# Optimization experiments

Hardware: AMD Instinct MI355X
Metric: run time of the kernel (lower is better)

## Reference

```python
import jax, jax.numpy as jnp
import numpy as np

H_DIM, HEAD_DIM, N_HEADS = 1024, 64, 16
B, S = 4, 2048

def phi(x):
    return jax.nn.elu(x) + 1.0

def setup_inputs() -> dict:
    key = jax.random.key(0)
    ks = jax.random.split(key, 14)
    std = 0.02
    inp = {
        'query': jax.random.normal(ks[0], (B, S, H_DIM), jnp.float32),
        'key':   jax.random.normal(ks[1], (B, S, H_DIM), jnp.float32),
        'value': jax.random.normal(ks[2], (B, S, H_DIM), jnp.float32),
        'beta':  jax.random.normal(ks[3], (B, S, H_DIM), jnp.float32),
        # torch nn.Linear convention: W is [out, in]
        'Wq': std * jax.random.normal(ks[4], (N_HEADS * HEAD_DIM, H_DIM), jnp.float32),
        'bq': jnp.zeros((N_HEADS * HEAD_DIM,), jnp.float32),
        'Wk': std * jax.random.normal(ks[5], (N_HEADS * HEAD_DIM, H_DIM), jnp.float32),
        'bk': jnp.zeros((N_HEADS * HEAD_DIM,), jnp.float32),
        'Wv': std * jax.random.normal(ks[6], (N_HEADS * HEAD_DIM, H_DIM), jnp.float32),
        'bv': jnp.zeros((N_HEADS * HEAD_DIM,), jnp.float32),
        'Wb': std * jax.random.normal(ks[7], (N_HEADS, H_DIM), jnp.float32),
        'bb': jnp.zeros((N_HEADS,), jnp.float32),
        'Wo': std * jax.random.normal(ks[8], (H_DIM, N_HEADS * HEAD_DIM), jnp.float32),
        'bo': jnp.zeros((H_DIM,), jnp.float32),
    }
    return inp

def reference(query, key, value, beta, Wq, bq, Wk, bk, Wv, bv, Wb, bb, Wo, bo):
    bsz, seqlen, _ = query.shape
    q = query @ Wq.T + bq            # [B,S,H*D]
    k = key   @ Wk.T + bk
    v = value @ Wv.T + bv
    b = jax.nn.sigmoid(beta @ Wb.T + bb)  # [B,S,H]

    def heads(x):  # [B,S,H*D] -> [B,H,S,D]
        return x.reshape(bsz, seqlen, N_HEADS, HEAD_DIM).transpose(0, 2, 1, 3)
    q, k, v = heads(q), heads(k), heads(v)
    b = b.transpose(0, 2, 1)              # [B,H,S]

    phi_q, phi_k = phi(q), phi(k)

    # NOTE: the original uses torch.einsum('bhdd,bhd->bhd', W, x), whose repeated
    # subscript takes the DIAGONAL of W. The recurrence thus reduces exactly to a
    # d-vector diagonal state: s <- s + beta*(v - s*pk)*pk ; y = s_new * pq.
    def step(s, xs):
        pk_t, pq_t, v_t, b_t = xs          # [B,H,D],[B,H,D],[B,H,D],[B,H]
        v_bar = s * pk_t                   # diag(prev_W) @ phi_k  == elementwise
        bdv = b_t[..., None] * (v_t - v_bar)
        s_new = s + bdv * pk_t             # diagonal of prev_W + outer(bdv, pk)
        y = s_new * pq_t                   # diag(curr_W) * phi_q
        return s_new, y

    # time-major scan inputs: [S,B,H,D]
    xs = (phi_k.transpose(2, 0, 1, 3), phi_q.transpose(2, 0, 1, 3),
          v.transpose(2, 0, 1, 3), b.transpose(2, 0, 1))
    s0 = jnp.zeros((bsz, N_HEADS, HEAD_DIM), query.dtype)
    _, ys = jax.lax.scan(step, s0, xs)     # ys: [S,B,H,D]

    out = ys.transpose(1, 0, 2, 3).reshape(bsz, seqlen, N_HEADS * HEAD_DIM)
    return out @ Wo.T + bo
```

## Files before the change

kernel.cpp:

```cpp
#include <hip/hip_runtime.h>
#include <cstdint>
#include <cstddef>

#define H_DIM 1024
#define HEADS 16
#define HD 64
#define BATCH 4
#define SEQ 2048
#define M_ROWS (BATCH*SEQ)

typedef __bf16 bf16x8 __attribute__((ext_vector_type(8)));
typedef float floatx4 __attribute__((ext_vector_type(4)));
typedef unsigned short ushortx8 __attribute__((ext_vector_type(8)));

__device__ __forceinline__ unsigned short f2bf(float f) {
    union { float f; uint32_t u; } c; c.f = f;
    uint32_t u = c.u;
    u += 0x7fffu + ((u >> 16) & 1u);
    return (unsigned short)(u >> 16);
}
__device__ __forceinline__ float bf2f(unsigned short h) {
    union { uint32_t u; float f; } c; c.u = ((uint32_t)h) << 16;
    return c.f;
}

#define GLD_LDS16(gp, lp) \
    __builtin_amdgcn_global_load_lds((__attribute__((address_space(1))) void*)(gp), \
                                     (__attribute__((address_space(3))) void*)(lp), 16, 0, 0)

__global__ __launch_bounds__(256) void cast_bf16(const float* __restrict__ in,
                                                 unsigned short* __restrict__ out)
{
    size_t i = (size_t)blockIdx.x * 256 + threadIdx.x;
    const float4* p = (const float4*)in;
    float4 a = p[i * 2], b = p[i * 2 + 1];
    ushortx8 o;
    o[0] = f2bf(a.x); o[1] = f2bf(a.y); o[2] = f2bf(a.z); o[3] = f2bf(a.w);
    o[4] = f2bf(b.x); o[5] = f2bf(b.y); o[6] = f2bf(b.z); o[7] = f2bf(b.w);
    *(ushortx8*)(out + i * 8) = o;
}

enum { EPI_NONE = 0, EPI_PHI = 1 };

__device__ __forceinline__ void store_out(float* C, size_t idx, float x) { C[idx] = x; }
__device__ __forceinline__ void store_out(unsigned short* C, size_t idx, float x) { C[idx] = f2bf(x); }

template<int EPI, typename OutT>
__global__ __launch_bounds__(256) void gemm_mfma(const unsigned short* __restrict__ A,
                                                 const unsigned short* __restrict__ W,
                                                 const float* __restrict__ bias,
                                                 OutT* __restrict__ C,
                                                 int M, int N, int K)
{
    constexpr int TM = 128, TN = 128, TK = 32;
    __shared__ __align__(16) unsigned short Ast[TM * TK];
    __shared__ __align__(16) unsigned short Bst[TN * TK];

    const int tid  = threadIdx.x;
    const int wave = tid >> 6;
    const int lane = tid & 63;
    const int bm = blockIdx.y * TM;
    const int bn = blockIdx.x * TN;

    const int srow  = wave * 16 + (lane >> 2);
    const int skoff = (lane & 3) * 8;

    const int wm   = (wave & 1) * 64;
    const int wn   = (wave >> 1) * 64;
    const int quad = lane >> 4;
    const int l16  = lane & 15;

    floatx4 acc[4][4] = {};

    const unsigned short* Abase = A + (size_t)bm * K;
    const unsigned short* Wbase = W + (size_t)bn * K;

    for (int k0 = 0; k0 < K; k0 += TK) {
        __syncthreads();
        GLD_LDS16(Abase + (size_t)srow        * K + k0 + skoff, &Ast[(wave * 16)      * TK]);
        GLD_LDS16(Abase + (size_t)(srow + 64) * K + k0 + skoff, &Ast[(64 + wave * 16) * TK]);
        GLD_LDS16(Wbase + (size_t)srow        * K + k0 + skoff, &Bst[(wave * 16)      * TK]);
        GLD_LDS16(Wbase + (size_t)(srow + 64) * K + k0 + skoff, &Bst[(64 + wave * 16) * TK]);
        __syncthreads();

        bf16x8 af[4], bfr[4];
        #pragma unroll
        for (int i = 0; i < 4; ++i)
            af[i] = *(const bf16x8*)&Ast[(wm + i * 16 + l16) * TK + quad * 8];
        #pragma unroll
        for (int j = 0; j < 4; ++j)
            bfr[j] = *(const bf16x8*)&Bst[(wn + j * 16 + l16) * TK + quad * 8];
        #pragma unroll
        for (int i = 0; i < 4; ++i)
            #pragma unroll
            for (int j = 0; j < 4; ++j)
                acc[i][j] = __builtin_amdgcn_mfma_f32_16x16x32_bf16(af[i], bfr[j], acc[i][j], 0, 0, 0);
    }

    #pragma unroll
    for (int i = 0; i < 4; ++i) {
        #pragma unroll
        for (int j = 0; j < 4; ++j) {
            const int col = bn + wn + j * 16 + l16;
            const float bval = bias[col];
            #pragma unroll
            for (int r = 0; r < 4; ++r) {
                const int row = bm + wm + i * 16 + quad * 4 + r;
                float x = acc[i][j][r] + bval;
                if (EPI == EPI_PHI) x = (x > 0.f) ? (x + 1.f) : __expf(x);
                store_out(C, (size_t)row * N + col, x);
            }
        }
    }
}

__global__ __launch_bounds__(256) void proj_b(const float* __restrict__ beta,
                                              const float* __restrict__ Wb,
                                              const float* __restrict__ bbias,
                                              float* __restrict__ bout)
{
    const int wave = threadIdx.x >> 6;
    const int lane = threadIdx.x & 63;
    const int m = blockIdx.x * 4 + wave;

    const float4* brow = (const float4*)(beta + (size_t)m * H_DIM);
    const float4* wb4  = (const float4*)Wb;

    float acc[16];
    #pragma unroll
    for (int n = 0; n < 16; ++n) acc[n] = 0.f;

    #pragma unroll
    for (int j = 0; j < 4; ++j) {
        float4 a = brow[j * 64 + lane];
        #pragma unroll
        for (int n = 0; n < 16; ++n) {
            float4 w = wb4[n * 256 + j * 64 + lane];
            acc[n] = fmaf(a.x, w.x, acc[n]);
            acc[n] = fmaf(a.y, w.y, acc[n]);
            acc[n] = fmaf(a.z, w.z, acc[n]);
            acc[n] = fmaf(a.w, w.w, acc[n]);
        }
    }

    #pragma unroll
    for (int n = 0; n < 16; ++n) {
        float s = acc[n];
        s += __shfl_xor(s, 32);
        s += __shfl_xor(s, 16);
        s += __shfl_xor(s, 8);
        s += __shfl_xor(s, 4);
        s += __shfl_xor(s, 2);
        s += __shfl_xor(s, 1);
        acc[n] = s;
    }

    float sel = acc[0];
    #pragma unroll
    for (int n = 1; n < 16; ++n)
        sel = (lane == n) ? acc[n] : sel;
    if (lane < 16) {
        float s = sel + bbias[lane];
        bout[(size_t)m * HEADS + lane] = 1.f / (1.f + __expf(-s));
    }
}

constexpr int NCHUNK = 64;
constexpr int CLEN   = SEQ / NCHUNK;
constexpr int NGH    = BATCH * HEADS * HD;

__global__ __launch_bounds__(256) void scan_phase1(const unsigned short* __restrict__ pk_,
                                                   const unsigned short* __restrict__ v_,
                                                   const float* __restrict__ b_,
                                                   float* __restrict__ Aarr,
                                                   float* __restrict__ Carr)
{
    const int idx   = blockIdx.x * 256 + threadIdx.x;
    const int d     = idx & 63;
    const int h     = (idx >> 6) & 15;
    const int bb    = (idx >> 10) & 3;
    const int chunk = idx >> 12;
    const int g     = idx & (NGH - 1);
    const int t0    = chunk * CLEN;

    const unsigned short* pkp = pk_ + (size_t)bb * SEQ * H_DIM + h * HD + d + (size_t)t0 * H_DIM;
    const unsigned short* vp  = v_  + (size_t)bb * SEQ * H_DIM + h * HD + d + (size_t)t0 * H_DIM;
    const float*          bp  = b_  + (size_t)bb * SEQ * HEADS + h        + (size_t)t0 * HEADS;

    float A = 1.f, C = 0.f;
    #pragma unroll 8
    for (int t = 0; t < CLEN; ++t) {
        float pk = bf2f(pkp[(size_t)t * H_DIM]);
        float vv = bf2f(vp[(size_t)t * H_DIM]);
        float bt = bp[(size_t)t * HEADS];
        float a  = 1.f - bt * pk * pk;
        float c  = bt * vv * pk;
        A *= a;
        C = fmaf(a, C, c);
    }
    Aarr[(size_t)chunk * NGH + g] = A;
    Carr[(size_t)chunk * NGH + g] = C;
}

__global__ __launch_bounds__(256) void scan_phase2(const float* __restrict__ Aarr,
                                                   const float* __restrict__ Carr,
                                                   float* __restrict__ S0)
{
    const int g = blockIdx.x * 256 + threadIdx.x;
    float s = 0.f;
    #pragma unroll
    for (int c = 0; c < NCHUNK; ++c) {
        S0[(size_t)c * NGH + g] = s;
        s = fmaf(Aarr[(size_t)c * NGH + g], s, Carr[(size_t)c * NGH + g]);
    }
}

__global__ __launch_bounds__(256) void scan_phase3(const unsigned short* __restrict__ pk_,
                                                   unsigned short* __restrict__ pq_,
                                                   const unsigned short* __restrict__ v_,
                                                   const float* __restrict__ b_,
                                                   const float* __restrict__ S0)
{
    const int idx   = blockIdx.x * 256 + threadIdx.x;
    const int d     = idx & 63;
    const int h     = (idx >> 6) & 15;
    const int bb    = (idx >> 10) & 3;
    const int chunk = idx >> 12;
    const int g     = idx & (NGH - 1);
    const int t0    = chunk * CLEN;

    const unsigned short* pkp = pk_ + (size_t)bb * SEQ * H_DIM + h * HD + d + (size_t)t0 * H_DIM;
    unsigned short*       pqp = pq_ + (size_t)bb * SEQ * H_DIM + h * HD + d + (size_t)t0 * H_DIM;
    const unsigned short* vp  = v_  + (size_t)bb * SEQ * H_DIM + h * HD + d + (size_t)t0 * H_DIM;
    const float*          bp  = b_  + (size_t)bb * SEQ * HEADS + h        + (size_t)t0 * HEADS;

    float s = S0[(size_t)chunk * NGH + g];
    #pragma unroll 8
    for (int t = 0; t < CLEN; ++t) {
        float pk = bf2f(pkp[(size_t)t * H_DIM]);
        float pq = bf2f(pqp[(size_t)t * H_DIM]);
        float vv = bf2f(vp[(size_t)t * H_DIM]);
        float bt = bp[(size_t)t * HEADS];
        float bdv = bt * (vv - s * pk);
        s = fmaf(bdv, pk, s);
        pqp[(size_t)t * H_DIM] = f2bf(s * pq);
    }
}

extern "C" void kernel_launch(void* const* d_in, const int* in_sizes, int n_in,
                              void* d_out, int out_size, void* d_ws, size_t ws_size,
                              hipStream_t stream)
{
    const float* query = (const float*)d_in[0];
    const float* key   = (const float*)d_in[1];
    const float* value = (const float*)d_in[2];
    const float* beta  = (const float*)d_in[3];
    const float* Wq    = (const float*)d_in[4];
    const float* bq    = (const float*)d_in[5];
    const float* Wk    = (const float*)d_in[6];
    const float* bk    = (const float*)d_in[7];
    const float* Wv    = (const float*)d_in[8];
    const float* bv    = (const float*)d_in[9];
    const float* Wb    = (const float*)d_in[10];
    const float* bbias = (const float*)d_in[11];
    const float* Wo    = (const float*)d_in[12];
    const float* bo    = (const float*)d_in[13];
    float* out = (float*)d_out;

    const size_t ACT = (size_t)M_ROWS * H_DIM;
    const size_t WEL = (size_t)H_DIM * H_DIM;

    unsigned short* ws = (unsigned short*)d_ws;
    unsigned short* Xbf    = ws;
    unsigned short* phi_q  = ws + ACT;
    unsigned short* phi_k  = ws + 2 * ACT;
    unsigned short* vbuf   = ws + 3 * ACT;
    unsigned short* Wq_bf  = ws + 4 * ACT;
    unsigned short* Wk_bf  = Wq_bf + WEL;
    unsigned short* Wv_bf  = Wk_bf + WEL;
    unsigned short* Wo_bf  = Wv_bf + WEL;
    float*          bbuf   = (float*)(Wo_bf + WEL);
    float*          Aarr   = bbuf + (size_t)M_ROWS * HEADS;
    float*          Carr   = Aarr + (size_t)NCHUNK * NGH;
    float*          S0     = Carr + (size_t)NCHUNK * NGH;

    const int ACT_CAST_BLOCKS = (int)(ACT / (8 * 256));
    const int W_CAST_BLOCKS   = (int)(WEL / (8 * 256));

    cast_bf16<<<W_CAST_BLOCKS, 256, 0, stream>>>(Wq, Wq_bf);
    cast_bf16<<<W_CAST_BLOCKS, 256, 0, stream>>>(Wk, Wk_bf);
    cast_bf16<<<W_CAST_BLOCKS, 256, 0, stream>>>(Wv, Wv_bf);
    cast_bf16<<<W_CAST_BLOCKS, 256, 0, stream>>>(Wo, Wo_bf);

    dim3 ggrid(H_DIM / 128, M_ROWS / 128);

    cast_bf16<<<ACT_CAST_BLOCKS, 256, 0, stream>>>(query, Xbf);
    gemm_mfma<EPI_PHI, unsigned short><<<ggrid, 256, 0, stream>>>(Xbf, Wq_bf, bq, phi_q, M_ROWS, H_DIM, H_DIM);
    cast_bf16<<<ACT_CAST_BLOCKS, 256, 0, stream>>>(key, Xbf);
    gemm_mfma<EPI_PHI, unsigned short><<<ggrid, 256, 0, stream>>>(Xbf, Wk_bf, bk, phi_k, M_ROWS, H_DIM, H_DIM);
    cast_bf16<<<ACT_CAST_BLOCKS, 256, 0, stream>>>(value, Xbf);
    gemm_mfma<EPI_NONE, unsigned short><<<ggrid, 256, 0, stream>>>(Xbf, Wv_bf, bv, vbuf, M_ROWS, H_DIM, H_DIM);

    proj_b<<<M_ROWS / 4, 256, 0, stream>>>(beta, Wb, bbias, bbuf);

    const int SCAN_BLOCKS = NGH * NCHUNK / 256;
    scan_phase1<<<SCAN_BLOCKS, 256, 0, stream>>>(phi_k, vbuf, bbuf, Aarr, Carr);
    scan_phase2<<<NGH / 256, 256, 0, stream>>>(Aarr, Carr, S0);
    scan_phase3<<<SCAN_BLOCKS, 256, 0, stream>>>(phi_k, phi_q, vbuf, bbuf, S0);

    gemm_mfma<EPI_NONE, float><<<ggrid, 256, 0, stream>>>(phi_q, Wo_bf, bo, out, M_ROWS, H_DIM, H_DIM);
}
```

Baseline: 384.4 us.

## Fuse activation casts into QKV GEMM, batch projections and prep kernels with XCD-aware tiling

Drops the separate fp32-to-bf16 activation cast kernels. The QKV GEMM now loads fp32 activations directly and converts them in registers before storing to LDS, and the three Q/K/V projections become a single launch with an XCD-aware block swizzle for L2 locality. The weight casts and the beta projection are merged into one prep launch, and the output GEMM uses 128x64 tiles with a swizzled grid to get more blocks. This saves several launches and the round trip of activations through bf16 in memory. In exchange, the A-operand loads become plain register loads instead of direct-to-LDS loads, and the GEMM issues more global traffic per k-step.

```diff
diff --git a/kernel.cpp b/kernel.cpp
--- a/kernel.cpp
+++ b/kernel.cpp
@@ -28,97 +28,34 @@
     __builtin_amdgcn_global_load_lds((__attribute__((address_space(1))) void*)(gp), \
                                      (__attribute__((address_space(3))) void*)(lp), 16, 0, 0)
 
-__global__ __launch_bounds__(256) void cast_bf16(const float* __restrict__ in,
-                                                 unsigned short* __restrict__ out)
-{
-    size_t i = (size_t)blockIdx.x * 256 + threadIdx.x;
-    const float4* p = (const float4*)in;
-    float4 a = p[i * 2], b = p[i * 2 + 1];
-    ushortx8 o;
-    o[0] = f2bf(a.x); o[1] = f2bf(a.y); o[2] = f2bf(a.z); o[3] = f2bf(a.w);
-    o[4] = f2bf(b.x); o[5] = f2bf(b.y); o[6] = f2bf(b.z); o[7] = f2bf(b.w);
-    *(ushortx8*)(out + i * 8) = o;
-}
-
-enum { EPI_NONE = 0, EPI_PHI = 1 };
-
-__device__ __forceinline__ void store_out(float* C, size_t idx, float x) { C[idx] = x; }
-__device__ __forceinline__ void store_out(unsigned short* C, size_t idx, float x) { C[idx] = f2bf(x); }
-
-template<int EPI, typename OutT>
-__global__ __launch_bounds__(256) void gemm_mfma(const unsigned short* __restrict__ A,
-                                                 const unsigned short* __restrict__ W,
-                                                 const float* __restrict__ bias,
-                                                 OutT* __restrict__ C,
-                                                 int M, int N, int K)
-{
-    constexpr int TM = 128, TN = 128, TK = 32;
-    __shared__ __align__(16) unsigned short Ast[TM * TK];
-    __shared__ __align__(16) unsigned short Bst[TN * TK];
-
-    const int tid  = threadIdx.x;
-    const int wave = tid >> 6;
-    const int lane = tid & 63;
-    const int bm = blockIdx.y * TM;
-    const int bn = blockIdx.x * TN;
-
-    const int srow  = wave * 16 + (lane >> 2);
-    const int skoff = (lane & 3) * 8;
-
-    const int wm   = (wave & 1) * 64;
-    const int wn   = (wave >> 1) * 64;
-    const int quad = lane >> 4;
-    const int l16  = lane & 15;
-
-    floatx4 acc[4][4] = {};
-
-    const unsigned short* Abase = A + (size_t)bm * K;
-    const unsigned short* Wbase = W + (size_t)bn * K;
-
-    for (int k0 = 0; k0 < K; k0 += TK) {
-        __syncthreads();
-        GLD_LDS16(Abase + (size_t)srow        * K + k0 + skoff, &Ast[(wave * 16)      * TK]);
-        GLD_LDS16(Abase + (size_t)(srow + 64) * K + k0 + skoff, &Ast[(64 + wave * 16) * TK]);
-        GLD_LDS16(Wbase + (size_t)srow        * K + k0 + skoff, &Bst[(wave * 16)      * TK]);
-        GLD_LDS16(Wbase + (size_t)(srow + 64) * K + k0 + skoff, &Bst[(64 + wave * 16) * TK]);
-        __syncthreads();
-
-        bf16x8 af[4], bfr[4];
-        #pragma unroll
-        for (int i = 0; i < 4; ++i)
-            af[i] = *(const bf16x8*)&Ast[(wm + i * 16 + l16) * TK + quad * 8];
-        #pragma unroll
-        for (int j = 0; j < 4; ++j)
-            bfr[j] = *(const bf16x8*)&Bst[(wn + j * 16 + l16) * TK + quad * 8];
-        #pragma unroll
-        for (int i = 0; i < 4; ++i)
-            #pragma unroll
-            for (int j = 0; j < 4; ++j)
-                acc[i][j] = __builtin_amdgcn_mfma_f32_16x16x32_bf16(af[i], bfr[j], acc[i][j], 0, 0, 0);
-    }
-
-    #pragma unroll
-    for (int i = 0; i < 4; ++i) {
-        #pragma unroll
-        for (int j = 0; j < 4; ++j) {
-            const int col = bn + wn + j * 16 + l16;
-            const float bval = bias[col];
-            #pragma unroll
-            for (int r = 0; r < 4; ++r) {
-                const int row = bm + wm + i * 16 + quad * 4 + r;
-                float x = acc[i][j][r] + bval;
-                if (EPI == EPI_PHI) x = (x > 0.f) ? (x + 1.f) : __expf(x);
-                store_out(C, (size_t)row * N + col, x);
-            }
-        }
-    }
-}
-
-__global__ __launch_bounds__(256) void proj_b(const float* __restrict__ beta,
-                                              const float* __restrict__ Wb,
-                                              const float* __restrict__ bbias,
-                                              float* __restrict__ bout)
-{
+__global__ __launch_bounds__(256) void prep(const float* __restrict__ Wq,
+                                            const float* __restrict__ Wk,
+                                            const float* __restrict__ Wv,
+                                            const float* __restrict__ Wo,
+                                            unsigned short* __restrict__ Wq_bf,
+                                            unsigned short* __restrict__ Wk_bf,
+                                            unsigned short* __restrict__ Wv_bf,
+                                            unsigned short* __restrict__ Wo_bf,
+                                            const float* __restrict__ beta,
+                                            const float* __restrict__ Wb,
+                                            const float* __restrict__ bbias,
+                                            float* __restrict__ bout)
+{
+    const int z = blockIdx.z;
+    if (z < 4) {
+        if (blockIdx.x >= 512) return;
+        const float* in = (z == 0) ? Wq : (z == 1) ? Wk : (z == 2) ? Wv : Wo;
+        unsigned short* out = (z == 0) ? Wq_bf : (z == 1) ? Wk_bf : (z == 2) ? Wv_bf : Wo_bf;
+        size_t i = (size_t)blockIdx.x * 256 + threadIdx.x;
+        const float4* p = (const float4*)in;
+        float4 a = p[i * 2], b = p[i * 2 + 1];
+        ushortx8 o;
+        o[0] = f2bf(a.x); o[1] = f2bf(a.y); o[2] = f2bf(a.z); o[3] = f2bf(a.w);
+        o[4] = f2bf(b.x); o[5] = f2bf(b.y); o[6] = f2bf(b.z); o[7] = f2bf(b.w);
+        *(ushortx8*)(out + i * 8) = o;
+        return;
+    }
+
     const int wave = threadIdx.x >> 6;
     const int lane = threadIdx.x & 63;
     const int m = blockIdx.x * 4 + wave;
@@ -162,6 +99,176 @@
     if (lane < 16) {
         float s = sel + bbias[lane];
         bout[(size_t)m * HEADS + lane] = 1.f / (1.f + __expf(-s));
+    }
+}
+
+__global__ __launch_bounds__(256) void gemm_qkv(const float* __restrict__ Aq,
+                                                const float* __restrict__ Ak,
+                                                const float* __restrict__ Av,
+                                                const unsigned short* __restrict__ Wqb,
+                                                const unsigned short* __restrict__ Wkb,
+                                                const unsigned short* __restrict__ Wvb,
+                                                const float* __restrict__ bq,
+                                                const float* __restrict__ bk,
+                                                const float* __restrict__ bv,
+                                                unsigned short* __restrict__ Cq,
+                                                unsigned short* __restrict__ Ck,
+                                                unsigned short* __restrict__ Cv)
+{
+    constexpr int TM = 128, TN = 128, TK = 32;
+    constexpr int K = H_DIM, N = H_DIM;
+    __shared__ __align__(16) unsigned short Ast[TM * TK];
+    __shared__ __align__(16) unsigned short Bst[TN * TK];
+
+    const int lin   = blockIdx.x;
+    const int xcd   = lin & 7;
+    const int ii    = lin >> 3;
+    const int panel = xcd * 24 + (ii >> 3);
+    const int nx    = ii & 7;
+    const int z     = panel >> 6;
+    const int my    = panel & 63;
+
+    const float* A          = (z == 0) ? Aq : (z == 1) ? Ak : Av;
+    const unsigned short* W = (z == 0) ? Wqb : (z == 1) ? Wkb : Wvb;
+    const float* bias       = (z == 0) ? bq : (z == 1) ? bk : bv;
+    unsigned short* C       = (z == 0) ? Cq : (z == 1) ? Ck : Cv;
+    const bool phi = (z < 2);
+
+    const int tid  = threadIdx.x;
+    const int wave = tid >> 6;
+    const int lane = tid & 63;
+    const int bm = my * TM;
+    const int bn = nx * TN;
+
+    const int srow  = wave * 16 + (lane >> 2);
+    const int skoff = (lane & 3) * 8;
+
+    const int wm   = (wave & 1) * 64;
+    const int wn   = (wave >> 1) * 64;
+    const int quad = lane >> 4;
+    const int l16  = lane & 15;
+
+    floatx4 acc[4][4] = {};
+
+    const float*          Abase = A + (size_t)bm * K;
+    const unsigned short* Wbase = W + (size_t)bn * K;
+
+    for (int k0 = 0; k0 < K; k0 += TK) {
+        __syncthreads();
+        GLD_LDS16(Wbase + (size_t)srow        * K + k0 + skoff, &Bst[(wave * 16)      * TK]);
+        GLD_LDS16(Wbase + (size_t)(srow + 64) * K + k0 + skoff, &Bst[(64 + wave * 16) * TK]);
+        float4 a0 = *(const float4*)&Abase[(size_t)srow        * K + k0 + skoff];
+        float4 a1 = *(const float4*)&Abase[(size_t)srow        * K + k0 + skoff + 4];
+        float4 a2 = *(const float4*)&Abase[(size_t)(srow + 64) * K + k0 + skoff];
+        float4 a3 = *(const float4*)&Abase[(size_t)(srow + 64) * K + k0 + skoff + 4];
+        ushortx8 w0, w1;
+        w0[0] = f2bf(a0.x); w0[1] = f2bf(a0.y); w0[2] = f2bf(a0.z); w0[3] = f2bf(a0.w);
+        w0[4] = f2bf(a1.x); w0[5] = f2bf(a1.y); w0[6] = f2bf(a1.z); w0[7] = f2bf(a1.w);
+        w1[0] = f2bf(a2.x); w1[1] = f2bf(a2.y); w1[2] = f2bf(a2.z); w1[3] = f2bf(a2.w);
+        w1[4] = f2bf(a3.x); w1[5] = f2bf(a3.y); w1[6] = f2bf(a3.z); w1[7] = f2bf(a3.w);
+        *(ushortx8*)&Ast[(size_t)srow        * TK + skoff] = w0;
+        *(ushortx8*)&Ast[(size_t)(srow + 64) * TK + skoff] = w1;
+        __syncthreads();
+
+        bf16x8 af[4], bfr[4];
+        #pragma unroll
+        for (int i = 0; i < 4; ++i)
+            af[i] = *(const bf16x8*)&Ast[(wm + i * 16 + l16) * TK + quad * 8];
+        #pragma unroll
+        for (int j = 0; j < 4; ++j)
+            bfr[j] = *(const bf16x8*)&Bst[(wn + j * 16 + l16) * TK + quad * 8];
+        #pragma unroll
+        for (int i = 0; i < 4; ++i)
+            #pragma unroll
+            for (int j = 0; j < 4; ++j)
+                acc[i][j] = __builtin_amdgcn_mfma_f32_16x16x32_bf16(af[i], bfr[j], acc[i][j], 0, 0, 0);
+    }
+
+    #pragma unroll
+    for (int i = 0; i < 4; ++i) {
+        #pragma unroll
+        for (int j = 0; j < 4; ++j) {
+            const int col = bn + wn + j * 16 + l16;
+            const float bval = bias[col];
+            #pragma unroll
+            for (int r = 0; r < 4; ++r) {
+                const int row = bm + wm + i * 16 + quad * 4 + r;
+                float x = acc[i][j][r] + bval;
+                if (phi) x = (x > 0.f) ? (x + 1.f) : __expf(x);
+                C[(size_t)row * N + col] = f2bf(x);
+            }
+        }
+    }
+}
+
+__global__ __launch_bounds__(256) void gemm_out(const unsigned short* __restrict__ A,
+                                                const unsigned short* __restrict__ W,
+                                                const float* __restrict__ bias,
+                                                float* __restrict__ C)
+{
+    constexpr int TM = 128, TN = 64, TK = 32;
+    constexpr int K = H_DIM, N = H_DIM;
+    __shared__ __align__(16) unsigned short Ast[TM * TK];
+    __shared__ __align__(16) unsigned short Bst[TN * TK];
+
+    const int lin = blockIdx.x;
+    const int xcd = lin & 7;
+    const int ii  = lin >> 3;
+    const int my  = xcd * 8 + (ii >> 4);
+    const int nx  = ii & 15;
+
+    const int tid  = threadIdx.x;
+    const int wave = tid >> 6;
+    const int lane = tid & 63;
+    const int bm = my * TM;
+    const int bn = nx * TN;
+
+    const int srow  = wave * 16 + (lane >> 2);
+    const int skoff = (lane & 3) * 8;
+
+    const int wm   = (wave & 1) * 64;
+    const int wn   = (wave >> 1) * 32;
+    const int quad = lane >> 4;
+    const int l16  = lane & 15;
+
+    floatx4 acc[4][2] = {};
+
+    const unsigned short* Abase = A + (size_t)bm * K;
+    const unsigned short* Wbase = W + (size_t)bn * K;
+
+    for (int k0 = 0; k0 < K; k0 += TK) {
+        __syncthreads();
+        GLD_LDS16(Abase + (size_t)srow        * K + k0 + skoff, &Ast[(wave * 16)      * TK]);
+        GLD_LDS16(Abase + (size_t)(srow + 64) * K + k0 + skoff, &Ast[(64 + wave * 16) * TK]);
+        GLD_LDS16(Wbase + (size_t)srow        * K + k0 + skoff, &Bst[(wave * 16)      * TK]);
+        __syncthreads();
+
+        bf16x8 af[4], bfr[2];
+        #pragma unroll
+        for (int i = 0; i < 4; ++i)
+            af[i] = *(const bf16x8*)&Ast[(wm + i * 16 + l16) * TK + quad * 8];
+        #pragma unroll
+        for (int j = 0; j < 2; ++j)
+            bfr[j] = *(const bf16x8*)&Bst[(wn + j * 16 + l16) * TK + quad * 8];
+        #pragma unroll
+        for (int i = 0; i < 4; ++i)
+            #pragma unroll
+            for (int j = 0; j < 2; ++j)
+                acc[i][j] = __builtin_amdgcn_mfma_f32_16x16x32_bf16(af[i], bfr[j], acc[i][j], 0, 0, 0);
+    }
+
+    #pragma unroll
+    for (int i = 0; i < 4; ++i) {
+        #pragma unroll
+        for (int j = 0; j < 2; ++j) {
+            const int col = bn + wn + j * 16 + l16;
+            const float bval = bias[col];
+            #pragma unroll
+            for (int r = 0; r < 4; ++r) {
+                const int row = bm + wm + i * 16 + quad * 4 + r;
+                C[(size_t)row * N + col] = acc[i][j][r] + bval;
+            }
+        }
     }
 }
 
@@ -271,11 +378,10 @@
     const size_t WEL = (size_t)H_DIM * H_DIM;
 
     unsigned short* ws = (unsigned short*)d_ws;
-    unsigned short* Xbf    = ws;
-    unsigned short* phi_q  = ws + ACT;
-    unsigned short* phi_k  = ws + 2 * ACT;
-    unsigned short* vbuf   = ws + 3 * ACT;
-    unsigned short* Wq_bf  = ws + 4 * ACT;
+    unsigned short* phi_q  = ws;
+    unsigned short* phi_k  = ws + ACT;
+    unsigned short* vbuf   = ws + 2 * ACT;
+    unsigned short* Wq_bf  = ws + 3 * ACT;
     unsigned short* Wk_bf  = Wq_bf + WEL;
     unsigned short* Wv_bf  = Wk_bf + WEL;
     unsigned short* Wo_bf  = Wv_bf + WEL;
@@ -284,29 +390,19 @@
     float*          Carr   = Aarr + (size_t)NCHUNK * NGH;
     float*          S0     = Carr + (size_t)NCHUNK * NGH;
 
-    const int ACT_CAST_BLOCKS = (int)(ACT / (8 * 256));
-    const int W_CAST_BLOCKS   = (int)(WEL / (8 * 256));
-
-    cast_bf16<<<W_CAST_BLOCKS, 256, 0, stream>>>(Wq, Wq_bf);
-    cast_bf16<<<W_CAST_BLOCKS, 256, 0, stream>>>(Wk, Wk_bf);
-    cast_bf16<<<W_CAST_BLOCKS, 256, 0, stream>>>(Wv, Wv_bf);
-    cast_bf16<<<W_CAST_BLOCKS, 256, 0, stream>>>(Wo, Wo_bf);
-
-    dim3 ggrid(H_DIM / 128, M_ROWS / 128);
-
-    cast_bf16<<<ACT_CAST_BLOCKS, 256, 0, stream>>>(query, Xbf);
-    gemm_mfma<EPI_PHI, unsigned short><<<ggrid, 256, 0, stream>>>(Xbf, Wq_bf, bq, phi_q, M_ROWS, H_DIM, H_DIM);
-    cast_bf16<<<ACT_CAST_BLOCKS, 256, 0, stream>>>(key, Xbf);
-    gemm_mfma<EPI_PHI, unsigned short><<<ggrid, 256, 0, stream>>>(Xbf, Wk_bf, bk, phi_k, M_ROWS, H_DIM, H_DIM);
-    cast_bf16<<<ACT_CAST_BLOCKS, 256, 0, stream>>>(value, Xbf);
-    gemm_mfma<EPI_NONE, unsigned short><<<ggrid, 256, 0, stream>>>(Xbf, Wv_bf, bv, vbuf, M_ROWS, H_DIM, H_DIM);
-
-    proj_b<<<M_ROWS / 4, 256, 0, stream>>>(beta, Wb, bbias, bbuf);
+    prep<<<dim3(2048, 1, 5), 256, 0, stream>>>(Wq, Wk, Wv, Wo,
+                                               Wq_bf, Wk_bf, Wv_bf, Wo_bf,
+                                               beta, Wb, bbias, bbuf);
+
+    gemm_qkv<<<1536, 256, 0, stream>>>(query, key, value,
+                                       Wq_bf, Wk_bf, Wv_bf,
+                                       bq, bk, bv,
+                                       phi_q, phi_k, vbuf);
 
     const int SCAN_BLOCKS = NGH * NCHUNK / 256;
     scan_phase1<<<SCAN_BLOCKS, 256, 0, stream>>>(phi_k, vbuf, bbuf, Aarr, Carr);
     scan_phase2<<<NGH / 256, 256, 0, stream>>>(Aarr, Carr, S0);
     scan_phase3<<<SCAN_BLOCKS, 256, 0, stream>>>(phi_k, phi_q, vbuf, bbuf, S0);
 
-    gemm_mfma<EPI_NONE, float><<<ggrid, 256, 0, stream>>>(phi_q, Wo_bf, bo, out, M_ROWS, H_DIM, H_DIM);
-}
+    gemm_out<<<1024, 256, 0, stream>>>(phi_q, Wo_bf, bo, out);
+}
```

Measured after the change: 365.1 us. 1.05x faster.
